# Kernel optimization log

Hardware: AMD Instinct MI355X
Metric: run time of the kernel (lower is better)

The kernel has to match this reference:

```python
import jax, jax.numpy as jnp
import numpy as np

N, E = 50000, 800000
NFEAT, NHID, NCLASS = 512, 256, 64
RRELU_SLOPE = (1.0 / 8.0 + 1.0 / 3.0) / 2.0  # nn.RReLU eval-mode negative slope


def spmm(row, col, val, X):
    # sparse adj (COO: row, col, val) @ dense X -> [N, F]
    return jax.ops.segment_sum(X[col] * val[:, None], row, num_segments=N)


def setup_inputs() -> dict:
    key = jax.random.key(0)
    ks = jax.random.split(key, 12)
    x = jax.random.normal(ks[0], (N, NFEAT), dtype=jnp.float32)
    edge_row = jnp.sort(jax.random.randint(ks[1], (E,), 0, N))
    edge_col = jax.random.randint(ks[2], (E,), 0, N)
    # normalized-ish positive adjacency values
    edge_val = jax.random.uniform(ks[3], (E,), dtype=jnp.float32) / 16.0
    def glorot(k, fi, fo):
        s = 1.0 / np.sqrt(fi)
        return jax.random.normal(k, (fi, fo), dtype=jnp.float32) * s
    w1 = glorot(ks[4], NFEAT, NHID)
    b1 = jax.random.normal(ks[5], (NHID,), dtype=jnp.float32) * 0.01
    w2 = glorot(ks[6], NFEAT, NHID)
    b2 = jax.random.normal(ks[7], (NHID,), dtype=jnp.float32) * 0.01
    w3 = glorot(ks[8], NHID, NCLASS)
    b3 = jax.random.normal(ks[9], (NCLASS,), dtype=jnp.float32) * 0.01
    w4 = glorot(ks[10], NFEAT, NCLASS)
    b4 = jax.random.normal(ks[11], (NCLASS,), dtype=jnp.float32) * 0.01
    return {"x": x, "edge_row": edge_row, "edge_col": edge_col, "edge_val": edge_val,
            "w1": w1, "b1": b1, "w2": w2, "b2": b2, "w3": w3, "b3": b3, "w4": w4, "b4": b4}


def reference(x, edge_row, edge_col, edge_val, w1, b1, w2, b2, w3, b3, w4, b4):
    # skip branches (no adj): support = x @ W + b; dropout is identity in eval
    a_skip0 = x @ w2 + b2                                   # [N, NHID]
    a_skip1 = x @ w4 + b4                                   # [N, NCLASS]
    # gc1 with adj
    h1 = spmm(edge_row, edge_col, edge_val, x @ w1) + b1    # [N, NHID]
    v = h1 + a_skip0
    h = jnp.where(v >= 0, v, v * RRELU_SLOPE)               # RReLU (eval mode)
    # gc3 with adj
    out = spmm(edge_row, edge_col, edge_val, h @ w3) + b3 + a_skip1  # [N, NCLASS]
    return (out, w1, w2, w3, w4)
```

## Files before the change

kernel.cpp:

```cpp
#include <hip/hip_runtime.h>

#define N_NODES 50000
#define N_EDGES 800000
#define NFEAT 512
#define NHID 256
#define NCLASS 64
#define NCOMB 576
#define NPAD 640
#define NSKIP 320
#define RRELU_SLOPE 0.2291666666666667f

typedef __attribute__((ext_vector_type(8))) short bf16x8;
typedef __attribute__((ext_vector_type(4))) float f32x4;
typedef __attribute__((ext_vector_type(2))) float f32x2;

#define GLOAD_LDS16(g, l)                                                      \
    __builtin_amdgcn_global_load_lds(                                          \
        (const __attribute__((address_space(1))) void*)(g),                    \
        (__attribute__((address_space(3))) void*)(l), 16, 0, 0)

__device__ __forceinline__ unsigned short f2bf(float f) {
    unsigned int x = __float_as_uint(f);
    unsigned int r = (x + 0x7fffu + ((x >> 16) & 1u)) >> 16;
    return (unsigned short)r;
}
__device__ __forceinline__ float bf2f(unsigned short u) {
    return __uint_as_float(((unsigned int)u) << 16);
}
__device__ __forceinline__ float bf_lo(unsigned int u) { return __uint_as_float(u << 16); }
__device__ __forceinline__ float bf_hi(unsigned int u) { return __uint_as_float(u & 0xffff0000u); }
__device__ __forceinline__ unsigned char f2fp8(float v) {
    return (unsigned char)__builtin_amdgcn_cvt_pk_fp8_f32(v, v, 0, false);
}

#define S0 6400000
#define S1 7200000
#define S2 7527680
#define S3 7577681
#define S4 7594065
#define S5 7594705
#define S6 7672529
#define PREP_BLOCKS ((S6 + 255) / 256)

__global__ __launch_bounds__(256)
void prep(const float* __restrict__ x, const int* __restrict__ erow,
          const int* __restrict__ ecol, const float* __restrict__ ev,
          const float* __restrict__ w1, const float* __restrict__ b1,
          const float* __restrict__ w2, const float* __restrict__ b2,
          const float* __restrict__ w3, const float* __restrict__ b3,
          const float* __restrict__ w4, const float* __restrict__ b4,
          unsigned short* __restrict__ xb, unsigned short* __restrict__ Bt,
          float* __restrict__ biasb, unsigned short* __restrict__ w3t,
          uint2* __restrict__ ep, int* __restrict__ rp,
          float* __restrict__ out) {
    int i = blockIdx.x * 256 + threadIdx.x;
    if (i >= S6) return;
    if (i < S0) {
        float4 v = ((const float4*)x)[i];
        ushort4 o;
        o.x = f2bf(v.x); o.y = f2bf(v.y); o.z = f2bf(v.z); o.w = f2bf(v.w);
        ((ushort4*)xb)[i] = o;
    } else if (i < S1) {
        int j = i - S0;
        uint2 e;
        e.x = (unsigned)ecol[j];
        e.y = __float_as_uint(ev[j]);
        ep[j] = e;
    } else if (i < S2) {
        int j = i - S1;
        int c = j >> 9;
        int k = j & 511;
        float v = 0.f;
        if (c < NHID)            v = w1[k * NHID + c];
        else if (c < 2 * NHID)   v = w2[k * NHID + (c - NHID)];
        else if (c < NCOMB)      v = w4[k * NCLASS + (c - 2 * NHID)];
        Bt[j] = f2bf(v);
    } else if (i < S3) {
        int n = i - S2;
        int lo = 0, hi = N_EDGES;
        while (lo < hi) {
            int mid = (lo + hi) >> 1;
            if (erow[mid] < n) lo = mid + 1; else hi = mid;
        }
        rp[n] = lo;
    } else if (i < S4) {
        int j = i - S3;
        int c = j >> 8;
        int k = j & 255;
        w3t[j] = f2bf(w3[k * NCLASS + c]);
    } else if (i < S5) {
        int b = i - S4;
        float v = 0.f;
        if (b >= NHID && b < 2 * NHID)       v = b1[b - NHID] + b2[b - NHID];
        else if (b >= 2 * NHID && b < NCOMB) v = b3[b - 2 * NHID] + b4[b - 2 * NHID];
        biasb[b] = v;
    } else {
        int j = i - S5;
        float4* o4 = (float4*)out;
        if (j < 32768)        o4[800000 + j] = ((const float4*)w1)[j];
        else if (j < 65536)   o4[832768 + (j - 32768)] = ((const float4*)w2)[j - 32768];
        else if (j < 69632)   o4[865536 + (j - 65536)] = ((const float4*)w3)[j - 65536];
        else                  o4[869632 + (j - 69632)] = ((const float4*)w4)[j - 69632];
    }
}

#define GBM 128
#define GBK 64
#define NCB0 5
#define NRP0 392

template <int BN, int MODE>
__global__ __launch_bounds__(256, 4)
void gemm_bf16(const unsigned short* __restrict__ A,
               const unsigned short* __restrict__ Bt,
               const float* __restrict__ bias,
               unsigned char* __restrict__ C8,
               unsigned short* __restrict__ skipb,
               int M, int K, int NC) {
    constexpr int CF = BN / 32;
    __shared__ unsigned short As[GBM * GBK];
    __shared__ unsigned short Bs[BN * GBK];
    int row0, col0;
    if (MODE == 0) {
        int b = blockIdx.x;
        int g = b / (8 * NCB0);
        int w = b % (8 * NCB0);
        int r = g * 8 + (w & 7);
        int c = w >> 3;
        if (r * GBM >= M) return;
        row0 = r * GBM;
        col0 = c * BN;
    } else {
        col0 = blockIdx.x * BN;
        row0 = blockIdx.y * GBM;
    }
    const int tid  = threadIdx.x;
    const int lane = tid & 63;
    const int wave = tid >> 6;
    const int wr = (wave >> 1) * 64;
    const int wc = (wave & 1) * (BN / 2);
    const int lm = lane & 15;
    const int l4 = lane >> 4;
    const int sw = lm & 7;

    const int sub  = lane >> 3;
    const int slot = lane & 7;
    const int goct = slot ^ sub;

    f32x4 acc[4][CF] = {};

    for (int k0 = 0; k0 < K; k0 += GBK) {
        #pragma unroll
        for (int p = 0; p < 4; ++p) {
            int chunk = wave * 4 + p;
            int gr = row0 + chunk * 8 + sub;
            if (gr > M - 1) gr = M - 1;
            GLOAD_LDS16(A + (size_t)gr * K + k0 + goct * 8, As + chunk * 512);
        }
        #pragma unroll
        for (int p = 0; p < BN / 32; ++p) {
            int chunk = wave * (BN / 32) + p;
            int rb = col0 + chunk * 8 + sub;
            GLOAD_LDS16(Bt + (size_t)rb * K + k0 + goct * 8, Bs + chunk * 512);
        }
        __syncthreads();

        #pragma unroll
        for (int kk8 = 0; kk8 < GBK / 8; kk8 += 4) {
            const int so = ((kk8 + l4) ^ sw) * 8;
            bf16x8 bfr[CF];
            #pragma unroll
            for (int j = 0; j < CF; ++j)
                bfr[j] = *(const bf16x8*)(Bs + (wc + j * 16 + lm) * 64 + so);
            #pragma unroll
            for (int i = 0; i < 4; ++i) {
                bf16x8 af = *(const bf16x8*)(As + (wr + i * 16 + lm) * 64 + so);
                #pragma unroll
                for (int j = 0; j < CF; ++j)
                    acc[i][j] = __builtin_amdgcn_mfma_f32_16x16x32_bf16(af, bfr[j], acc[i][j], 0, 0, 0);
            }
        }
        __syncthreads();
    }

    #pragma unroll
    for (int i = 0; i < 4; ++i) {
        #pragma unroll
        for (int j = 0; j < CF; ++j) {
            int col = col0 + wc + j * 16 + lm;
            float bvv = (MODE == 0) ? bias[col] : 0.f;
            #pragma unroll
            for (int r = 0; r < 4; ++r) {
                int row = row0 + wr + i * 16 + l4 * 4 + r;
                if (row < M) {
                    float v = acc[i][j][r];
                    if (MODE == 0) {
                        if (col < NHID)       C8[(size_t)row * NHID + col] = f2fp8(v);
                        else if (col < NCOMB) skipb[(size_t)row * NSKIP + (col - NHID)] = f2bf(v + bvv);
                    } else {
                        C8[(size_t)row * NC + col] = f2fp8(v);
                    }
                }
            }
        }
    }
}

__global__ __launch_bounds__(256)
void spmm1_rrelu(const int* __restrict__ rp, const uint2* __restrict__ ep,
                 const unsigned char* __restrict__ xw1q,
                 const unsigned short* __restrict__ skipb,
                 unsigned short* __restrict__ hb, int n_nodes) {
    int n = blockIdx.x * 4 + (threadIdx.x >> 6);
    if (n >= n_nodes) return;
    int lane = threadIdx.x & 63;
    int f = lane * 4;
    int lo = rp[n], hi = rp[n + 1];
    float s0 = 0.f, s1 = 0.f, s2 = 0.f, s3 = 0.f;
    int e = lo;
    for (; e + 7 < hi; e += 8) {
        uint2 ed[8];
        unsigned p[8];
        #pragma unroll
        for (int q = 0; q < 8; ++q) ed[q] = ep[e + q];
        #pragma unroll
        for (int q = 0; q < 8; ++q)
            p[q] = *(const unsigned*)(xw1q + (size_t)ed[q].x * NHID + f);
        #pragma unroll
        for (int q = 0; q < 8; ++q) {
            float v = __uint_as_float(ed[q].y);
            f32x2 ab = __builtin_amdgcn_cvt_pk_f32_fp8((int)p[q], false);
            f32x2 cd = __builtin_amdgcn_cvt_pk_f32_fp8((int)p[q], true);
            s0 += v * ab.x;
            s1 += v * ab.y;
            s2 += v * cd.x;
            s3 += v * cd.y;
        }
    }
    for (; e < hi; ++e) {
        uint2 ee = ep[e];
        float v = __uint_as_float(ee.y);
        unsigned p = *(const unsigned*)(xw1q + (size_t)ee.x * NHID + f);
        f32x2 ab = __builtin_amdgcn_cvt_pk_f32_fp8((int)p, false);
        f32x2 cd = __builtin_amdgcn_cvt_pk_f32_fp8((int)p, true);
        s0 += v * ab.x;
        s1 += v * ab.y;
        s2 += v * cd.x;
        s3 += v * cd.y;
    }
    ushort4 sk = *(const ushort4*)(skipb + (size_t)n * NSKIP + f);
    float v0 = s0 + bf2f(sk.x), v1 = s1 + bf2f(sk.y);
    float v2 = s2 + bf2f(sk.z), v3 = s3 + bf2f(sk.w);
    v0 = (v0 >= 0.f) ? v0 : v0 * RRELU_SLOPE;
    v1 = (v1 >= 0.f) ? v1 : v1 * RRELU_SLOPE;
    v2 = (v2 >= 0.f) ? v2 : v2 * RRELU_SLOPE;
    v3 = (v3 >= 0.f) ? v3 : v3 * RRELU_SLOPE;
    ushort4 o;
    o.x = f2bf(v0); o.y = f2bf(v1); o.z = f2bf(v2); o.w = f2bf(v3);
    *(ushort4*)(hb + (size_t)n * NHID + f) = o;
}

__global__ __launch_bounds__(256)
void spmm2_out(const int* __restrict__ rp, const uint2* __restrict__ ep,
               const unsigned char* __restrict__ hw3q,
               const unsigned short* __restrict__ skipb,
               float* __restrict__ out, int n_nodes) {
    int n = blockIdx.x * 4 + (threadIdx.x >> 6);
    if (n >= n_nodes) return;
    int lane = threadIdx.x & 63;
    int q = lane >> 4;
    int l = lane & 15;
    int f = l * 4;
    int lo = rp[n], hi = rp[n + 1];
    float s0 = 0.f, s1 = 0.f, s2 = 0.f, s3 = 0.f;
    int e = lo + q;
    for (; e + 4 < hi; e += 8) {
        uint2 ea = ep[e], eb = ep[e + 4];
        unsigned pa = *(const unsigned*)(hw3q + (size_t)ea.x * NCLASS + f);
        unsigned pb = *(const unsigned*)(hw3q + (size_t)eb.x * NCLASS + f);
        float va = __uint_as_float(ea.y), vb = __uint_as_float(eb.y);
        f32x2 a0 = __builtin_amdgcn_cvt_pk_f32_fp8((int)pa, false);
        f32x2 a1 = __builtin_amdgcn_cvt_pk_f32_fp8((int)pa, true);
        f32x2 b0 = __builtin_amdgcn_cvt_pk_f32_fp8((int)pb, false);
        f32x2 b1 = __builtin_amdgcn_cvt_pk_f32_fp8((int)pb, true);
        s0 += va * a0.x + vb * b0.x;
        s1 += va * a0.y + vb * b0.y;
        s2 += va * a1.x + vb * b1.x;
        s3 += va * a1.y + vb * b1.y;
    }
    for (; e < hi; e += 4) {
        uint2 ee = ep[e];
        unsigned p = *(const unsigned*)(hw3q + (size_t)ee.x * NCLASS + f);
        float v = __uint_as_float(ee.y);
        f32x2 ab = __builtin_amdgcn_cvt_pk_f32_fp8((int)p, false);
        f32x2 cd = __builtin_amdgcn_cvt_pk_f32_fp8((int)p, true);
        s0 += v * ab.x;
        s1 += v * ab.y;
        s2 += v * cd.x;
        s3 += v * cd.y;
    }
    s0 += __shfl_xor(s0, 16); s0 += __shfl_xor(s0, 32);
    s1 += __shfl_xor(s1, 16); s1 += __shfl_xor(s1, 32);
    s2 += __shfl_xor(s2, 16); s2 += __shfl_xor(s2, 32);
    s3 += __shfl_xor(s3, 16); s3 += __shfl_xor(s3, 32);
    if (q == 0) {
        uint2 sv = *(const uint2*)(skipb + (size_t)n * NSKIP + NHID + f);
        float4 o;
        o.x = s0 + bf_lo(sv.x);
        o.y = s1 + bf_hi(sv.x);
        o.z = s2 + bf_lo(sv.y);
        o.w = s3 + bf_hi(sv.y);
        *(float4*)(out + (size_t)n * NCLASS + f) = o;
    }
}

extern "C" void kernel_launch(void* const* d_in, const int* in_sizes, int n_in,
                              void* d_out, int out_size, void* d_ws, size_t ws_size,
                              hipStream_t stream) {
    const float* x    = (const float*)d_in[0];
    const int*   erow = (const int*)d_in[1];
    const int*   ecol = (const int*)d_in[2];
    const float* ev   = (const float*)d_in[3];
    const float* w1   = (const float*)d_in[4];
    const float* b1   = (const float*)d_in[5];
    const float* w2   = (const float*)d_in[6];
    const float* b2   = (const float*)d_in[7];
    const float* w3   = (const float*)d_in[8];
    const float* b3   = (const float*)d_in[9];
    const float* w4   = (const float*)d_in[10];
    const float* b4   = (const float*)d_in[11];
    float* out = (float*)d_out;

    char* ws = (char*)d_ws;
    size_t off = 0;
    auto alloc = [&](size_t bytes) -> void* {
        off = (off + 255) & ~(size_t)255;
        void* p = ws + off;
        off += bytes;
        return p;
    };

    unsigned short* xb    = (unsigned short*)alloc((size_t)N_NODES * NFEAT * 2);
    unsigned short* Bt    = (unsigned short*)alloc((size_t)NFEAT * NPAD * 2);
    float*          biasb = (float*)alloc(NPAD * 4);
    unsigned char*  xw1q  = (unsigned char*)alloc((size_t)N_NODES * NHID);
    unsigned short* skipb = (unsigned short*)alloc((size_t)N_NODES * NSKIP * 2);
    unsigned short* hb    = (unsigned short*)alloc((size_t)N_NODES * NHID * 2);
    unsigned short* w3t   = (unsigned short*)alloc((size_t)NHID * NCLASS * 2);
    unsigned char*  hw3q  = (unsigned char*)alloc((size_t)N_NODES * NCLASS);
    int*            rp    = (int*)alloc((size_t)(N_NODES + 1) * 4);
    uint2*          ep    = (uint2*)alloc((size_t)N_EDGES * 8);

    prep<<<PREP_BLOCKS, 256, 0, stream>>>(x, erow, ecol, ev, w1, b1, w2, b2, w3, b3,
                                          w4, b4, xb, Bt, biasb, w3t, ep, rp, out);

    gemm_bf16<128, 0><<<NRP0 * NCB0, 256, 0, stream>>>(xb, Bt, biasb, xw1q, skipb,
                                                       N_NODES, NFEAT, NPAD);

    spmm1_rrelu<<<(N_NODES + 3) / 4, 256, 0, stream>>>(rp, ep, xw1q, skipb, hb, N_NODES);

    dim3 g2(NCLASS / 64, (N_NODES + GBM - 1) / GBM);
    gemm_bf16<64, 1><<<g2, 256, 0, stream>>>(hb, w3t, nullptr, hw3q, nullptr,
                                             N_NODES, NHID, NCLASS);

    spmm2_out<<<(N_NODES + 3) / 4, 256, 0, stream>>>(rp, ep, hw3q, skipb, out, N_NODES);
}
```

Measured before the change: 305.5 us.

## Fuse x fp32-to-bf16 conversion into GEMM load and move edge prep into GEMM tail blocks

New measurement: 298.7 us. 1.02x faster.

```diff
diff --git a/kernel.cpp b/kernel.cpp
--- a/kernel.cpp
+++ b/kernel.cpp
@@ -33,74 +33,32 @@
     return (unsigned char)__builtin_amdgcn_cvt_pk_fp8_f32(v, v, 0, false);
 }
 
-#define S0 6400000
-#define S1 7200000
-#define S2 7527680
-#define S3 7577681
-#define S4 7594065
-#define S5 7594705
-#define S6 7672529
-#define PREP_BLOCKS ((S6 + 255) / 256)
+#define P_BT 327680
+#define P_TOT 328320
+#define PREP_BLOCKS ((P_TOT + 255) / 256)
 
 __global__ __launch_bounds__(256)
-void prep(const float* __restrict__ x, const int* __restrict__ erow,
-          const int* __restrict__ ecol, const float* __restrict__ ev,
-          const float* __restrict__ w1, const float* __restrict__ b1,
-          const float* __restrict__ w2, const float* __restrict__ b2,
-          const float* __restrict__ w3, const float* __restrict__ b3,
-          const float* __restrict__ w4, const float* __restrict__ b4,
-          unsigned short* __restrict__ xb, unsigned short* __restrict__ Bt,
-          float* __restrict__ biasb, unsigned short* __restrict__ w3t,
-          uint2* __restrict__ ep, int* __restrict__ rp,
-          float* __restrict__ out) {
+void prep(const float* __restrict__ w1, const float* __restrict__ w2,
+          const float* __restrict__ w4, const float* __restrict__ b1,
+          const float* __restrict__ b2, const float* __restrict__ b3,
+          const float* __restrict__ b4, unsigned short* __restrict__ Bt,
+          float* __restrict__ biasb) {
     int i = blockIdx.x * 256 + threadIdx.x;
-    if (i >= S6) return;
-    if (i < S0) {
-        float4 v = ((const float4*)x)[i];
-        ushort4 o;
-        o.x = f2bf(v.x); o.y = f2bf(v.y); o.z = f2bf(v.z); o.w = f2bf(v.w);
-        ((ushort4*)xb)[i] = o;
-    } else if (i < S1) {
-        int j = i - S0;
-        uint2 e;
-        e.x = (unsigned)ecol[j];
-        e.y = __float_as_uint(ev[j]);
-        ep[j] = e;
-    } else if (i < S2) {
-        int j = i - S1;
-        int c = j >> 9;
-        int k = j & 511;
+    if (i >= P_TOT) return;
+    if (i < P_BT) {
+        int c = i >> 9;
+        int k = i & 511;
         float v = 0.f;
         if (c < NHID)            v = w1[k * NHID + c];
         else if (c < 2 * NHID)   v = w2[k * NHID + (c - NHID)];
         else if (c < NCOMB)      v = w4[k * NCLASS + (c - 2 * NHID)];
-        Bt[j] = f2bf(v);
-    } else if (i < S3) {
-        int n = i - S2;
-        int lo = 0, hi = N_EDGES;
-        while (lo < hi) {
-            int mid = (lo + hi) >> 1;
-            if (erow[mid] < n) lo = mid + 1; else hi = mid;
-        }
-        rp[n] = lo;
-    } else if (i < S4) {
-        int j = i - S3;
-        int c = j >> 8;
-        int k = j & 255;
-        w3t[j] = f2bf(w3[k * NCLASS + c]);
-    } else if (i < S5) {
-        int b = i - S4;
+        Bt[i] = f2bf(v);
+    } else {
+        int b = i - P_BT;
         float v = 0.f;
         if (b >= NHID && b < 2 * NHID)       v = b1[b - NHID] + b2[b - NHID];
         else if (b >= 2 * NHID && b < NCOMB) v = b3[b - 2 * NHID] + b4[b - 2 * NHID];
         biasb[b] = v;
-    } else {
-        int j = i - S5;
-        float4* o4 = (float4*)out;
-        if (j < 32768)        o4[800000 + j] = ((const float4*)w1)[j];
-        else if (j < 65536)   o4[832768 + (j - 32768)] = ((const float4*)w2)[j - 32768];
-        else if (j < 69632)   o4[865536 + (j - 65536)] = ((const float4*)w3)[j - 65536];
-        else                  o4[869632 + (j - 69632)] = ((const float4*)w4)[j - 69632];
     }
 }
 
@@ -108,21 +66,62 @@
 #define GBK 64
 #define NCB0 5
 #define NRP0 392
+#define T0 800000
+#define T1 850001
+#define T2 866385
+#define T3 944209
+#define TAIL_BLOCKS ((T3 + 255) / 256)
 
 template <int BN, int MODE>
 __global__ __launch_bounds__(256, 4)
-void gemm_bf16(const unsigned short* __restrict__ A,
+void gemm_bf16(const void* __restrict__ Araw,
                const unsigned short* __restrict__ Bt,
                const float* __restrict__ bias,
                unsigned char* __restrict__ C8,
                unsigned short* __restrict__ skipb,
-               int M, int K, int NC) {
+               int M, int K, int NC,
+               const int* __restrict__ erow, const int* __restrict__ ecol,
+               const float* __restrict__ ev, const float* __restrict__ w1f,
+               const float* __restrict__ w2f, const float* __restrict__ w3f,
+               const float* __restrict__ w4f, uint2* __restrict__ ep,
+               int* __restrict__ rp, unsigned short* __restrict__ w3t,
+               float* __restrict__ outw) {
     constexpr int CF = BN / 32;
     __shared__ unsigned short As[GBM * GBK];
     __shared__ unsigned short Bs[BN * GBK];
     int row0, col0;
     if (MODE == 0) {
         int b = blockIdx.x;
+        if (b >= NRP0 * NCB0) {
+            int i = (b - NRP0 * NCB0) * 256 + threadIdx.x;
+            if (i < T0) {
+                uint2 e;
+                e.x = (unsigned)ecol[i];
+                e.y = __float_as_uint(ev[i]);
+                ep[i] = e;
+            } else if (i < T1) {
+                int n = i - T0;
+                int lo = 0, hi = N_EDGES;
+                while (lo < hi) {
+                    int mid = (lo + hi) >> 1;
+                    if (erow[mid] < n) lo = mid + 1; else hi = mid;
+                }
+                rp[n] = lo;
+            } else if (i < T2) {
+                int j = i - T1;
+                int c = j >> 8;
+                int k = j & 255;
+                w3t[j] = f2bf(w3f[k * NCLASS + c]);
+            } else if (i < T3) {
+                int j = i - T2;
+                float4* o4 = (float4*)outw;
+                if (j < 32768)        o4[800000 + j] = ((const float4*)w1f)[j];
+                else if (j < 65536)   o4[832768 + (j - 32768)] = ((const float4*)w2f)[j - 32768];
+                else if (j < 69632)   o4[865536 + (j - 65536)] = ((const float4*)w3f)[j - 65536];
+                else                  o4[869632 + (j - 69632)] = ((const float4*)w4f)[j - 69632];
+            }
+            return;
+        }
         int g = b / (8 * NCB0);
         int w = b % (8 * NCB0);
         int r = g * 8 + (w & 7);
@@ -150,18 +149,51 @@
     f32x4 acc[4][CF] = {};
 
     for (int k0 = 0; k0 < K; k0 += GBK) {
-        #pragma unroll
-        for (int p = 0; p < 4; ++p) {
-            int chunk = wave * 4 + p;
-            int gr = row0 + chunk * 8 + sub;
-            if (gr > M - 1) gr = M - 1;
-            GLOAD_LDS16(A + (size_t)gr * K + k0 + goct * 8, As + chunk * 512);
-        }
-        #pragma unroll
-        for (int p = 0; p < BN / 32; ++p) {
-            int chunk = wave * (BN / 32) + p;
-            int rb = col0 + chunk * 8 + sub;
-            GLOAD_LDS16(Bt + (size_t)rb * K + k0 + goct * 8, Bs + chunk * 512);
+        if (MODE == 0) {
+            const float* Ax = (const float*)Araw;
+            float4 fl[8];
+            #pragma unroll
+            for (int p = 0; p < 4; ++p) {
+                int chunk = wave * 4 + p;
+                int gr = row0 + chunk * 8 + sub;
+                if (gr > M - 1) gr = M - 1;
+                const float4* g = (const float4*)(Ax + (size_t)gr * K + k0 + goct * 8);
+                fl[2 * p]     = g[0];
+                fl[2 * p + 1] = g[1];
+            }
+            #pragma unroll
+            for (int p = 0; p < BN / 32; ++p) {
+                int chunk = wave * (BN / 32) + p;
+                int rb = col0 + chunk * 8 + sub;
+                GLOAD_LDS16(Bt + (size_t)rb * K + k0 + goct * 8, Bs + chunk * 512);
+            }
+            #pragma unroll
+            for (int p = 0; p < 4; ++p) {
+                unsigned c0, c1, c2, c3;
+                asm("v_cvt_pk_bf16_f32 %0, %1, %2" : "=v"(c0) : "v"(fl[2*p].x),     "v"(fl[2*p].y));
+                asm("v_cvt_pk_bf16_f32 %0, %1, %2" : "=v"(c1) : "v"(fl[2*p].z),     "v"(fl[2*p].w));
+                asm("v_cvt_pk_bf16_f32 %0, %1, %2" : "=v"(c2) : "v"(fl[2*p+1].x),   "v"(fl[2*p+1].y));
+                asm("v_cvt_pk_bf16_f32 %0, %1, %2" : "=v"(c3) : "v"(fl[2*p+1].z),   "v"(fl[2*p+1].w));
+                uint4 pk;
+                pk.x = c0; pk.y = c1; pk.z = c2; pk.w = c3;
+                int chunk = wave * 4 + p;
+                *((uint4*)(As + chunk * 512) + lane) = pk;
+            }
+        } else {
+            const unsigned short* A = (const unsigned short*)Araw;
+            #pragma unroll
+            for (int p = 0; p < 4; ++p) {
+                int chunk = wave * 4 + p;
+                int gr = row0 + chunk * 8 + sub;
+                if (gr > M - 1) gr = M - 1;
+                GLOAD_LDS16(A + (size_t)gr * K + k0 + goct * 8, As + chunk * 512);
+            }
+            #pragma unroll
+            for (int p = 0; p < BN / 32; ++p) {
+                int chunk = wave * (BN / 32) + p;
+                int rb = col0 + chunk * 8 + sub;
+                GLOAD_LDS16(Bt + (size_t)rb * K + k0 + goct * 8, Bs + chunk * 512);
+            }
         }
         __syncthreads();
 
@@ -340,7 +372,6 @@
         return p;
     };
 
-    unsigned short* xb    = (unsigned short*)alloc((size_t)N_NODES * NFEAT * 2);
     unsigned short* Bt    = (unsigned short*)alloc((size_t)NFEAT * NPAD * 2);
     float*          biasb = (float*)alloc(NPAD * 4);
     unsigned char*  xw1q  = (unsigned char*)alloc((size_t)N_NODES * NHID);
@@ -351,17 +382,20 @@
     int*            rp    = (int*)alloc((size_t)(N_NODES + 1) * 4);
     uint2*          ep    = (uint2*)alloc((size_t)N_EDGES * 8);
 
-    prep<<<PREP_BLOCKS, 256, 0, stream>>>(x, erow, ecol, ev, w1, b1, w2, b2, w3, b3,
-                                          w4, b4, xb, Bt, biasb, w3t, ep, rp, out);
-
-    gemm_bf16<128, 0><<<NRP0 * NCB0, 256, 0, stream>>>(xb, Bt, biasb, xw1q, skipb,
-                                                       N_NODES, NFEAT, NPAD);
+    prep<<<PREP_BLOCKS, 256, 0, stream>>>(w1, w2, w4, b1, b2, b3, b4, Bt, biasb);
+
+    gemm_bf16<128, 0><<<NRP0 * NCB0 + TAIL_BLOCKS, 256, 0, stream>>>(
+        x, Bt, biasb, xw1q, skipb, N_NODES, NFEAT, NPAD,
+        erow, ecol, ev, w1, w2, w3, w4, ep, rp, w3t, out);
 
     spmm1_rrelu<<<(N_NODES + 3) / 4, 256, 0, stream>>>(rp, ep, xw1q, skipb, hb, N_NODES);
 
     dim3 g2(NCLASS / 64, (N_NODES + GBM - 1) / GBM);
     gemm_bf16<64, 1><<<g2, 256, 0, stream>>>(hb, w3t, nullptr, hw3q, nullptr,
-                                             N_NODES, NHID, NCLASS);
+                                             N_NODES, NHID, NCLASS,
+                                             nullptr, nullptr, nullptr, nullptr,
+                                             nullptr, nullptr, nullptr, nullptr,
+                                             nullptr, nullptr, nullptr);
 
     spmm2_out<<<(N_NODES + 3) / 4, 256, 0, stream>>>(rp, ep, hw3q, skipb, out, N_NODES);
 }
```
